# Kernel optimization log

Hardware: AMD Instinct MI355X
Metric: run time of the kernel (lower is better)

Reference implementation:

```python
import jax, jax.numpy as jnp
import numpy as np
from jax import lax

HIDDEN = 16
DN = ('NCHW', 'OIHW', 'NCHW')

def setup_inputs() -> dict:
    key = jax.random.key(0)
    k1, k2, k3 = jax.random.split(key, 3)
    b, t, c, h, w = 8, 12, 5, 256, 256
    x = jax.random.normal(k1, (b, t, c, h, w), dtype=jnp.float32)
    # PyTorch-like init scale for conv weights
    W_cell = jax.random.normal(k2, (4 * HIDDEN, c + HIDDEN, 3, 3), dtype=jnp.float32) * 0.05
    b_cell = jnp.zeros((4 * HIDDEN,), dtype=jnp.float32)
    W_final = jax.random.normal(k3, (1, HIDDEN, 1, 1), dtype=jnp.float32) * 0.1
    b_final = jnp.zeros((1,), dtype=jnp.float32)
    return {"x": x, "W_cell": W_cell, "b_cell": b_cell,
            "W_final": W_final, "b_final": b_final}

def _cell_step(h_c, x_t, W_cell, b_cell):
    h_cur, c_cur = h_c
    combined = jnp.concatenate([x_t, h_cur], axis=1)          # [B, C+H, H, W]
    conv = lax.conv_general_dilated(combined, W_cell, (1, 1), 'SAME',
                                    dimension_numbers=DN)
    conv = conv + b_cell[None, :, None, None]                  # [B, 4H, H, W]
    cc_i, cc_f, cc_o, cc_g = jnp.split(conv, 4, axis=1)
    i = jax.nn.sigmoid(cc_i)
    f = jax.nn.sigmoid(cc_f)
    o = jax.nn.sigmoid(cc_o)
    g = jnp.tanh(cc_g)
    c_next = f * c_cur + i * g
    h_next = o * jnp.tanh(c_next)
    return h_next, c_next

def reference(x, W_cell, b_cell, W_final, b_final):
    b, t, c, hh, ww = x.shape
    h0 = jnp.zeros((b, HIDDEN, hh, ww), dtype=x.dtype)
    c0 = jnp.zeros((b, HIDDEN, hh, ww), dtype=x.dtype)
    xt = jnp.moveaxis(x, 1, 0)  # [T, B, C, H, W] for scan over time

    def step(carry, x_t):
        return _cell_step(carry, x_t, W_cell, b_cell), None

    (h_last, _), _ = lax.scan(step, (h0, c0), xt)
    out = lax.conv_general_dilated(h_last, W_final, (1, 1), 'SAME',
                                   dimension_numbers=DN)
    out = out + b_final[None, :, None, None]
    return out
```

## Files before the change

kernel.cpp:

```cpp
#include <hip/hip_runtime.h>
#include <math.h>

#define HIDDEN 16
#define CIN 5
#define BB 8
#define TT 12
#define HH 256
#define WW 256
#define TX 32
#define TY 8
#define HALO_X 34
#define HALO_Y 10
#define NPX (HALO_X * HALO_Y)
#define STRIDE 40

typedef __attribute__((ext_vector_type(8))) short bf16x8;
typedef __attribute__((ext_vector_type(4))) float floatx4;

__device__ __forceinline__ unsigned short f2bf(float f) {
    unsigned int u = __float_as_uint(f);
    u += 0x7fffu + ((u >> 16) & 1u);
    return (unsigned short)(u >> 16);
}
__device__ __forceinline__ float bf2f(unsigned short s) {
    return __uint_as_float(((unsigned int)s) << 16);
}
__device__ __forceinline__ float fast_sigmoid(float x) { return 1.0f / (1.0f + __expf(-x)); }
__device__ __forceinline__ float fast_tanh(float x) {
    float e2 = __expf(-2.0f * fabsf(x));
    float t = (1.0f - e2) / (1.0f + e2);
    return copysignf(t, x);
}

__global__ void prep_w_kernel(const float* __restrict__ Wc,
                              unsigned short* __restrict__ Wfrag) {
    int i = blockIdx.x * 256 + threadIdx.x;
    if (i >= 9 * 4 * 64 * 8) return;
    int j    = i & 7;
    int lane = (i >> 3) & 63;
    int g    = (i >> 9) & 3;
    int tap  = i >> 11;
    int k    = ((lane >> 4) << 3) + j;
    int col  = lane & 15;
    int o    = g * 16 + col;
    float w  = 0.0f;
    if (k < 21) {
        int ci_ref = (k < 16) ? (5 + k) : (k - 16);
        w = Wc[(o * 21 + ci_ref) * 9 + tap];
    }
    Wfrag[i] = f2bf(w);
}

__global__ void prep_x_kernel(const float* __restrict__ x,
                              unsigned short* __restrict__ xp) {
    size_t n = (size_t)blockIdx.x * 256 + threadIdx.x;
    const size_t TOTPX = (size_t)BB * TT * HH * WW;
    if (n >= TOTPX) return;
    size_t bt  = n / (size_t)(HH * WW);
    size_t pix = n - bt * (size_t)(HH * WW);
    const float* src = x + bt * (size_t)CIN * HH * WW + pix;
    unsigned short v[8];
    #pragma unroll
    for (int c = 0; c < CIN; ++c) v[c] = f2bf(src[(size_t)c * HH * WW]);
    v[5] = 0; v[6] = 0; v[7] = 0;
    *(uint4*)&xp[n * 8] = *(const uint4*)v;
}

__global__ __launch_bounds__(256, 5)
void convlstm_step_kernel(const float* __restrict__ x, int t,
                          const unsigned short* __restrict__ xp,
                          const unsigned short* __restrict__ h_in,
                          unsigned short* __restrict__ h_out,
                          float* __restrict__ c_state,
                          const unsigned short* __restrict__ Wfrag,
                          const float* __restrict__ bias,
                          int first, int use_xp) {
    __shared__ unsigned short tile[NPX * STRIDE];

    const int tid  = threadIdx.x;
    const int lane = tid & 63;
    const int wave = tid >> 6;
    const int x0 = blockIdx.x * TX;
    const int y0 = blockIdx.y * TY;
    const int bb = blockIdx.z;

    for (int i = tid; i < NPX; i += 256) {
        int ly = i / HALO_X;
        int lx = i - ly * HALO_X;
        int gy = y0 + ly - 1;
        int gx = x0 + lx - 1;
        bool inb = (gy >= 0 && gy < HH && gx >= 0 && gx < WW);
        unsigned short* row = &tile[i * STRIDE];
        uint4 z = {0, 0, 0, 0};
        if (inb && !first) {
            size_t hb = ((size_t)bb * HH * WW + (size_t)gy * WW + gx) * HIDDEN;
            *(uint4*)&row[0] = *(const uint4*)&h_in[hb];
            *(uint4*)&row[8] = *(const uint4*)&h_in[hb + 8];
        } else {
            *(uint4*)&row[0] = z;
            *(uint4*)&row[8] = z;
        }
        if (use_xp) {
            if (inb) {
                size_t xb = (((size_t)bb * TT + t) * (size_t)(HH * WW)
                             + (size_t)gy * WW + gx) * 8;
                *(uint4*)&row[16] = *(const uint4*)&xp[xb];
            } else {
                *(uint4*)&row[16] = z;
            }
        } else {
            #pragma unroll
            for (int ci = 0; ci < CIN; ++ci) {
                float v = 0.0f;
                if (inb) v = x[(((size_t)bb * TT + t) * CIN + ci) * (size_t)(HH * WW)
                               + (size_t)gy * WW + gx];
                row[16 + ci] = f2bf(v);
            }
            row[21] = 0; row[22] = 0; row[23] = 0;
        }
        *(uint4*)&row[24] = z;
    }
    __syncthreads();

    const int u    = lane & 15;
    const int quad = lane >> 4;

    float bg[4];
    #pragma unroll
    for (int g = 0; g < 4; ++g) bg[g] = bias[g * 16 + u];

    #pragma unroll 1
    for (int half = 0; half < 2; ++half) {
        floatx4 acc[2][4];
        int abase[2];
        #pragma unroll
        for (int mh = 0; mh < 2; ++mh) {
            int ml = half * 2 + mh;
            int m  = wave + ml * 4;
            int my = m >> 1;
            int mx = (m & 1) << 4;
            abase[mh] = (my * HALO_X + mx + u) * STRIDE + quad * 8;
            #pragma unroll
            for (int g = 0; g < 4; ++g)
                acc[mh][g] = (floatx4){bg[g], bg[g], bg[g], bg[g]};
        }

        #pragma unroll 3
        for (int tap = 0; tap < 9; ++tap) {
            int ky = tap / 3;
            int kx = tap - ky * 3;
            int toff = (ky * HALO_X + kx) * STRIDE;
            bf16x8 bfr[4];
            #pragma unroll
            for (int g = 0; g < 4; ++g)
                bfr[g] = *(const bf16x8*)&Wfrag[(size_t)((tap * 4 + g) * 64 + lane) * 8];
            #pragma unroll
            for (int mh = 0; mh < 2; ++mh) {
                bf16x8 af = *(const bf16x8*)&tile[abase[mh] + toff];
                #pragma unroll
                for (int g = 0; g < 4; ++g)
                    acc[mh][g] = __builtin_amdgcn_mfma_f32_16x16x32_bf16(
                        af, bfr[g], acc[mh][g], 0, 0, 0);
            }
        }

        #pragma unroll
        for (int mh = 0; mh < 2; ++mh) {
            int ml = half * 2 + mh;
            int m  = wave + ml * 4;
            int my = m >> 1;
            int mx = (m & 1) << 4;
            int py = y0 + my;
            #pragma unroll
            for (int r = 0; r < 4; ++r) {
                int pxx = x0 + mx + quad * 4 + r;
                size_t idx = ((size_t)bb * HH * WW + (size_t)py * WW + pxx) * HIDDEN + u;
                float ig = fast_sigmoid(acc[mh][0][r]);
                float fg = fast_sigmoid(acc[mh][1][r]);
                float og = fast_sigmoid(acc[mh][2][r]);
                float gg = fast_tanh(acc[mh][3][r]);
                float c_old = first ? 0.0f : c_state[idx];
                float c_new = fg * c_old + ig * gg;
                c_state[idx] = c_new;
                h_out[idx] = f2bf(og * fast_tanh(c_new));
            }
        }
    }
}

__global__ void final_conv_kernel(const unsigned short* __restrict__ h,
                                  const float* __restrict__ Wf,
                                  const float* __restrict__ bf_,
                                  float* __restrict__ out) {
    int i = blockIdx.x * 256 + threadIdx.x;
    if (i >= BB * HH * WW) return;
    size_t base = (size_t)i * HIDDEN;
    uint4 v0 = *(const uint4*)&h[base];
    uint4 v1 = *(const uint4*)&h[base + 8];
    const unsigned short* p0 = (const unsigned short*)&v0;
    const unsigned short* p1 = (const unsigned short*)&v1;
    float s = bf_[0];
    #pragma unroll
    for (int k = 0; k < 8; ++k) s += Wf[k] * bf2f(p0[k]);
    #pragma unroll
    for (int k = 0; k < 8; ++k) s += Wf[8 + k] * bf2f(p1[k]);
    out[i] = s;
}

extern "C" void kernel_launch(void* const* d_in, const int* in_sizes, int n_in,
                              void* d_out, int out_size, void* d_ws, size_t ws_size,
                              hipStream_t stream) {
    const float* x  = (const float*)d_in[0];
    const float* Wc = (const float*)d_in[1];
    const float* bc = (const float*)d_in[2];
    const float* Wf = (const float*)d_in[3];
    const float* bf = (const float*)d_in[4];
    float* out = (float*)d_out;

    char* ws = (char*)d_ws;
    const size_t h_bytes = (size_t)BB * HH * WW * HIDDEN * 2;
    const size_t c_bytes = (size_t)BB * HH * WW * HIDDEN * 4;
    const size_t w_bytes = 9 * 4 * 64 * 8 * 2;
    const size_t x_bytes = (size_t)BB * TT * HH * WW * 8 * 2;

    unsigned short* h_a = (unsigned short*)(ws);
    unsigned short* h_b = (unsigned short*)(ws + h_bytes);
    float* c            = (float*)(ws + 2 * h_bytes);
    unsigned short* Wfr = (unsigned short*)(ws + 2 * h_bytes + c_bytes);
    unsigned short* xp  = (unsigned short*)(ws + 2 * h_bytes + c_bytes + w_bytes);

    const int use_xp =
        (ws_size >= 2 * h_bytes + c_bytes + w_bytes + x_bytes) ? 1 : 0;

    prep_w_kernel<<<(9 * 4 * 64 * 8 + 255) / 256, 256, 0, stream>>>(Wc, Wfr);
    if (use_xp) {
        size_t totpx = (size_t)BB * TT * HH * WW;
        prep_x_kernel<<<(int)((totpx + 255) / 256), 256, 0, stream>>>(x, xp);
    }

    dim3 grid(WW / TX, HH / TY, BB);
    dim3 block(256, 1, 1);

    const unsigned short* h_in = h_a;
    for (int t = 0; t < TT; ++t) {
        unsigned short* h_out = (t & 1) ? h_b : h_a;
        convlstm_step_kernel<<<grid, block, 0, stream>>>(
            x, t, use_xp ? xp : (const unsigned short*)0,
            h_in, h_out, c, Wfr, bc, (t == 0) ? 1 : 0, use_xp);
        h_in = h_out;
    }

    final_conv_kernel<<<(BB * HH * WW + 255) / 256, 256, 0, stream>>>(
        h_in, Wf, bf, out);
}
```

Measured before the change: 695.9 us.

## Pack conv K dimension across taps to cut MFMA count from 9 to 7

Repacks the implicit-GEMM reduction so each 32-wide MFMA K slice spans two taps of hidden channels (16 each) or several taps of the 5 input channels, instead of one tap padded from 21 to 32. This drops the per-tile MFMA count per output group from 9 to 7 and removes wasted zero-padded K lanes. The cost is irregular per-quad LDS offsets, including one special slot at offset 70*STRIDE that is meant to point at a zero region. Both the weight packing and the A-fragment addressing must match exactly for the result to stay correct.

```diff
diff --git a/kernel.cpp b/kernel.cpp
--- a/kernel.cpp
+++ b/kernel.cpp
@@ -13,6 +13,7 @@
 #define HALO_Y 10
 #define NPX (HALO_X * HALO_Y)
 #define STRIDE 40
+#define NMFMA 7
 
 typedef __attribute__((ext_vector_type(8))) short bf16x8;
 typedef __attribute__((ext_vector_type(4))) float floatx4;
@@ -35,18 +36,25 @@
 __global__ void prep_w_kernel(const float* __restrict__ Wc,
                               unsigned short* __restrict__ Wfrag) {
     int i = blockIdx.x * 256 + threadIdx.x;
-    if (i >= 9 * 4 * 64 * 8) return;
+    if (i >= NMFMA * 4 * 64 * 8) return;
     int j    = i & 7;
     int lane = (i >> 3) & 63;
     int g    = (i >> 9) & 3;
-    int tap  = i >> 11;
+    int mi   = i >> 11;
     int k    = ((lane >> 4) << 3) + j;
     int col  = lane & 15;
     int o    = g * 16 + col;
+    int slot = 2 * mi + (k >> 4);
+    int w16  = k & 15;
     float w  = 0.0f;
-    if (k < 21) {
-        int ci_ref = (k < 16) ? (5 + k) : (k - 16);
-        w = Wc[(o * 21 + ci_ref) * 9 + tap];
+    if (slot <= 8) {
+        w = Wc[(o * 21 + 5 + w16) * 9 + slot];
+    } else {
+        int pair = slot - 9;
+        int xt   = pair * 2 + (w16 >> 3);
+        int ch   = w16 & 7;
+        if (xt < 9 && ch < 5)
+            w = Wc[(o * 21 + ch) * 9 + xt];
     }
     Wfrag[i] = f2bf(w);
 }
@@ -125,6 +133,20 @@
     const int u    = lane & 15;
     const int quad = lane >> 4;
 
+    int aoff[NMFMA];
+    #pragma unroll
+    for (int s = 0; s < 4; ++s) {
+        int tap = s * 2 + (quad >> 1);
+        aoff[s] = ((tap / 3) * HALO_X + (tap % 3)) * STRIDE + (quad & 1) * 8;
+    }
+    aoff[4] = (quad < 2) ? (70 * STRIDE + quad * 8)
+                         : ((quad - 2) * STRIDE + 16);
+    { int t5 = 2 + quad;
+      aoff[5] = ((t5 / 3) * HALO_X + (t5 % 3)) * STRIDE + 16; }
+    { int t6 = (quad == 3) ? 8 : (6 + quad);
+      int of6 = (quad == 3) ? 24 : 16;
+      aoff[6] = ((t6 / 3) * HALO_X + (t6 % 3)) * STRIDE + of6; }
+
     float bg[4];
     #pragma unroll
     for (int g = 0; g < 4; ++g) bg[g] = bias[g * 16 + u];
@@ -139,24 +161,21 @@
             int m  = wave + ml * 4;
             int my = m >> 1;
             int mx = (m & 1) << 4;
-            abase[mh] = (my * HALO_X + mx + u) * STRIDE + quad * 8;
+            abase[mh] = (my * HALO_X + mx + u) * STRIDE;
             #pragma unroll
             for (int g = 0; g < 4; ++g)
                 acc[mh][g] = (floatx4){bg[g], bg[g], bg[g], bg[g]};
         }
 
-        #pragma unroll 3
-        for (int tap = 0; tap < 9; ++tap) {
-            int ky = tap / 3;
-            int kx = tap - ky * 3;
-            int toff = (ky * HALO_X + kx) * STRIDE;
+        #pragma unroll
+        for (int mi = 0; mi < NMFMA; ++mi) {
             bf16x8 bfr[4];
             #pragma unroll
             for (int g = 0; g < 4; ++g)
-                bfr[g] = *(const bf16x8*)&Wfrag[(size_t)((tap * 4 + g) * 64 + lane) * 8];
+                bfr[g] = *(const bf16x8*)&Wfrag[(size_t)((mi * 4 + g) * 64 + lane) * 8];
             #pragma unroll
             for (int mh = 0; mh < 2; ++mh) {
-                bf16x8 af = *(const bf16x8*)&tile[abase[mh] + toff];
+                bf16x8 af = *(const bf16x8*)&tile[abase[mh] + aoff[mi]];
                 #pragma unroll
                 for (int g = 0; g < 4; ++g)
                     acc[mh][g] = __builtin_amdgcn_mfma_f32_16x16x32_bf16(
@@ -220,7 +239,7 @@
     char* ws = (char*)d_ws;
     const size_t h_bytes = (size_t)BB * HH * WW * HIDDEN * 2;
     const size_t c_bytes = (size_t)BB * HH * WW * HIDDEN * 4;
-    const size_t w_bytes = 9 * 4 * 64 * 8 * 2;
+    const size_t w_bytes = NMFMA * 4 * 64 * 8 * 2;
     const size_t x_bytes = (size_t)BB * TT * HH * WW * 8 * 2;
 
     unsigned short* h_a = (unsigned short*)(ws);
@@ -232,7 +251,7 @@
     const int use_xp =
         (ws_size >= 2 * h_bytes + c_bytes + w_bytes + x_bytes) ? 1 : 0;
 
-    prep_w_kernel<<<(9 * 4 * 64 * 8 + 255) / 256, 256, 0, stream>>>(Wc, Wfr);
+    prep_w_kernel<<<(NMFMA * 4 * 64 * 8 + 255) / 256, 256, 0, stream>>>(Wc, Wfr);
     if (use_xp) {
         size_t totpx = (size_t)BB * TT * HH * WW;
         prep_x_kernel<<<(int)((totpx + 255) / 256), 256, 0, stream>>>(x, xp);
```

Result: slower. 1.665 ms (+139.2%).

## Fuse all timesteps into a persistent cooperative kernel with register-resident cell state

Applied to the files above, without the earlier changes.

Replaces the twelve per-timestep launches and the final conv launch with one cooperative persistent kernel. It runs 1024 blocks that each own two tiles, keeps the cell state c in registers across timesteps, and uses grid.sync between steps. The final 1x1 conv is fused into the last step through a shuffle reduction. This removes launch gaps and the global c-state reads and writes, at the cost of grid-wide barriers, lower occupancy (launch bounds 4), and more register pressure from the eight-float cell arrays per tile.

```diff
diff --git a/kernel.cpp b/kernel.cpp
--- a/kernel.cpp
+++ b/kernel.cpp
@@ -1,4 +1,5 @@
 #include <hip/hip_runtime.h>
+#include <hip/hip_cooperative_groups.h>
 #include <math.h>
 
 #define HIDDEN 16
@@ -13,9 +14,12 @@
 #define HALO_Y 10
 #define NPX (HALO_X * HALO_Y)
 #define STRIDE 40
+#define NBLK_PERSIST 1024
 
 typedef __attribute__((ext_vector_type(8))) short bf16x8;
 typedef __attribute__((ext_vector_type(4))) float floatx4;
+
+namespace cg = cooperative_groups;
 
 __device__ __forceinline__ unsigned short f2bf(float f) {
     unsigned int u = __float_as_uint(f);
@@ -66,6 +70,169 @@
     *(uint4*)&xp[n * 8] = *(const uint4*)v;
 }
 
+__global__ __launch_bounds__(256, 4)
+void convlstm_persistent_kernel(const float* __restrict__ x,
+                                const unsigned short* __restrict__ xp,
+                                unsigned short* __restrict__ ha,
+                                unsigned short* __restrict__ hbuf,
+                                const unsigned short* __restrict__ Wfrag,
+                                const float* __restrict__ bias,
+                                const float* __restrict__ Wf,
+                                const float* __restrict__ bfin,
+                                float* __restrict__ out,
+                                int use_xp) {
+    __shared__ unsigned short tile[NPX * STRIDE];
+    cg::grid_group grid = cg::this_grid();
+
+    const int tid  = threadIdx.x;
+    const int lane = tid & 63;
+    const int wave = tid >> 6;
+    const int u    = lane & 15;
+    const int quad = lane >> 4;
+
+    float bg[4];
+    #pragma unroll
+    for (int g = 0; g < 4; ++g) bg[g] = bias[g * 16 + u];
+    const float wfu = Wf[u];
+    const float bf0 = bfin[0];
+
+    float cA[2][2][4];
+    float cB[2][2][4];
+    #pragma unroll
+    for (int a = 0; a < 2; ++a)
+        #pragma unroll
+        for (int m = 0; m < 2; ++m)
+            #pragma unroll
+            for (int r = 0; r < 4; ++r) { cA[a][m][r] = 0.0f; cB[a][m][r] = 0.0f; }
+
+    #pragma unroll 1
+    for (int t = 0; t < TT; ++t) {
+        const unsigned short* h_in  = (t & 1) ? ha : hbuf;
+        unsigned short*       h_out = (t & 1) ? hbuf : ha;
+        const int first = (t == 0);
+        const int last  = (t == TT - 1);
+
+        #pragma unroll
+        for (int tl = 0; tl < 2; ++tl) {
+            const int n  = (int)blockIdx.x + tl * NBLK_PERSIST;
+            const int x0 = (n & 7) * TX;
+            const int y0 = ((n >> 3) & 31) * TY;
+            const int bb = n >> 8;
+
+            if (t > 0 || tl > 0) __syncthreads();
+
+            for (int i = tid; i < NPX; i += 256) {
+                int ly = i / HALO_X;
+                int lx = i - ly * HALO_X;
+                int gy = y0 + ly - 1;
+                int gx = x0 + lx - 1;
+                bool inb = (gy >= 0 && gy < HH && gx >= 0 && gx < WW);
+                unsigned short* row = &tile[i * STRIDE];
+                uint4 z = {0, 0, 0, 0};
+                if (inb && !first) {
+                    size_t hbase = ((size_t)bb * HH * WW + (size_t)gy * WW + gx) * HIDDEN;
+                    *(uint4*)&row[0] = *(const uint4*)&h_in[hbase];
+                    *(uint4*)&row[8] = *(const uint4*)&h_in[hbase + 8];
+                } else {
+                    *(uint4*)&row[0] = z;
+                    *(uint4*)&row[8] = z;
+                }
+                if (use_xp) {
+                    if (inb) {
+                        size_t xb = (((size_t)bb * TT + t) * (size_t)(HH * WW)
+                                     + (size_t)gy * WW + gx) * 8;
+                        *(uint4*)&row[16] = *(const uint4*)&xp[xb];
+                    } else {
+                        *(uint4*)&row[16] = z;
+                    }
+                } else {
+                    #pragma unroll
+                    for (int ci = 0; ci < CIN; ++ci) {
+                        float v = 0.0f;
+                        if (inb) v = x[(((size_t)bb * TT + t) * CIN + ci) * (size_t)(HH * WW)
+                                       + (size_t)gy * WW + gx];
+                        row[16 + ci] = f2bf(v);
+                    }
+                    row[21] = 0; row[22] = 0; row[23] = 0;
+                }
+                *(uint4*)&row[24] = z;
+            }
+            __syncthreads();
+
+            #pragma unroll 1
+            for (int half = 0; half < 2; ++half) {
+                floatx4 acc[2][4];
+                int abase[2];
+                #pragma unroll
+                for (int mh = 0; mh < 2; ++mh) {
+                    int ml = half * 2 + mh;
+                    int m  = wave + ml * 4;
+                    int my = m >> 1;
+                    int mx = (m & 1) << 4;
+                    abase[mh] = (my * HALO_X + mx + u) * STRIDE + quad * 8;
+                    #pragma unroll
+                    for (int g = 0; g < 4; ++g)
+                        acc[mh][g] = (floatx4){bg[g], bg[g], bg[g], bg[g]};
+                }
+
+                #pragma unroll 3
+                for (int tap = 0; tap < 9; ++tap) {
+                    int ky = tap / 3;
+                    int kx = tap - ky * 3;
+                    int toff = (ky * HALO_X + kx) * STRIDE;
+                    bf16x8 bfr[4];
+                    #pragma unroll
+                    for (int g = 0; g < 4; ++g)
+                        bfr[g] = *(const bf16x8*)&Wfrag[(size_t)((tap * 4 + g) * 64 + lane) * 8];
+                    #pragma unroll
+                    for (int mh = 0; mh < 2; ++mh) {
+                        bf16x8 af = *(const bf16x8*)&tile[abase[mh] + toff];
+                        #pragma unroll
+                        for (int g = 0; g < 4; ++g)
+                            acc[mh][g] = __builtin_amdgcn_mfma_f32_16x16x32_bf16(
+                                af, bfr[g], acc[mh][g], 0, 0, 0);
+                    }
+                }
+
+                #pragma unroll
+                for (int mh = 0; mh < 2; ++mh) {
+                    int ml = half * 2 + mh;
+                    int m  = wave + ml * 4;
+                    int my = m >> 1;
+                    int mx = (m & 1) << 4;
+                    int py = y0 + my;
+                    #pragma unroll
+                    for (int r = 0; r < 4; ++r) {
+                        int pxx = x0 + mx + quad * 4 + r;
+                        float ig = fast_sigmoid(acc[mh][0][r]);
+                        float fg = fast_sigmoid(acc[mh][1][r]);
+                        float og = fast_sigmoid(acc[mh][2][r]);
+                        float gg = fast_tanh(acc[mh][3][r]);
+                        float c_old = half ? cB[tl][mh][r] : cA[tl][mh][r];
+                        float c_new = fg * c_old + ig * gg;
+                        if (half) cB[tl][mh][r] = c_new; else cA[tl][mh][r] = c_new;
+                        float hval = og * fast_tanh(c_new);
+                        if (last) {
+                            float s = wfu * hval;
+                            s += __shfl_xor(s, 1);
+                            s += __shfl_xor(s, 2);
+                            s += __shfl_xor(s, 4);
+                            s += __shfl_xor(s, 8);
+                            if (u == 0)
+                                out[(size_t)bb * HH * WW + (size_t)py * WW + pxx] = s + bf0;
+                        } else {
+                            size_t idx = ((size_t)bb * HH * WW + (size_t)py * WW + pxx)
+                                         * HIDDEN + u;
+                            h_out[idx] = f2bf(hval);
+                        }
+                    }
+                }
+            }
+        }
+        if (t != TT - 1) grid.sync();
+    }
+}
+
 __global__ __launch_bounds__(256, 5)
 void convlstm_step_kernel(const float* __restrict__ x, int t,
                           const unsigned short* __restrict__ xp,
@@ -93,9 +260,9 @@
         unsigned short* row = &tile[i * STRIDE];
         uint4 z = {0, 0, 0, 0};
         if (inb && !first) {
-            size_t hb = ((size_t)bb * HH * WW + (size_t)gy * WW + gx) * HIDDEN;
-            *(uint4*)&row[0] = *(const uint4*)&h_in[hb];
-            *(uint4*)&row[8] = *(const uint4*)&h_in[hb + 8];
+            size_t hbase = ((size_t)bb * HH * WW + (size_t)gy * WW + gx) * HIDDEN;
+            *(uint4*)&row[0] = *(const uint4*)&h_in[hbase];
+            *(uint4*)&row[8] = *(const uint4*)&h_in[hbase + 8];
         } else {
             *(uint4*)&row[0] = z;
             *(uint4*)&row[8] = z;
@@ -238,18 +405,36 @@
         prep_x_kernel<<<(int)((totpx + 255) / 256), 256, 0, stream>>>(x, xp);
     }
 
-    dim3 grid(WW / TX, HH / TY, BB);
-    dim3 block(256, 1, 1);
-
-    const unsigned short* h_in = h_a;
-    for (int t = 0; t < TT; ++t) {
-        unsigned short* h_out = (t & 1) ? h_b : h_a;
-        convlstm_step_kernel<<<grid, block, 0, stream>>>(
-            x, t, use_xp ? xp : (const unsigned short*)0,
-            h_in, h_out, c, Wfr, bc, (t == 0) ? 1 : 0, use_xp);
-        h_in = h_out;
-    }
-
-    final_conv_kernel<<<(BB * HH * WW + 255) / 256, 256, 0, stream>>>(
-        h_in, Wf, bf, out);
-}
+    int occ = 0;
+    hipOccupancyMaxActiveBlocksPerMultiprocessor(&occ, convlstm_persistent_kernel,
+                                                 256, 0);
+    bool done = false;
+    if (occ >= 4) {
+        const unsigned short* xp_arg = use_xp ? xp : (const unsigned short*)0;
+        int use_xp_arg = use_xp;
+        void* kargs[] = {
+            (void*)&x, (void*)&xp_arg, (void*)&h_a, (void*)&h_b,
+            (void*)&Wfr, (void*)&bc, (void*)&Wf, (void*)&bf,
+            (void*)&out, (void*)&use_xp_arg
+        };
+        if (hipLaunchCooperativeKernel((const void*)convlstm_persistent_kernel,
+                                       dim3(NBLK_PERSIST, 1, 1), dim3(256, 1, 1),
+                                       kargs, 0, stream) == hipSuccess)
+            done = true;
+    }
+
+    if (!done) {
+        dim3 grid(WW / TX, HH / TY, BB);
+        dim3 block(256, 1, 1);
+        const unsigned short* h_in = h_a;
+        for (int t = 0; t < TT; ++t) {
+            unsigned short* h_out = (t & 1) ? h_b : h_a;
+            convlstm_step_kernel<<<grid, block, 0, stream>>>(
+                x, t, use_xp ? xp : (const unsigned short*)0,
+                h_in, h_out, c, Wfr, bc, (t == 0) ? 1 : 0, use_xp);
+            h_in = h_out;
+        }
+        final_conv_kernel<<<(BB * HH * WW + 255) / 256, 256, 0, stream>>>(
+            h_in, Wf, bf, out);
+    }
+}
```

New measurement: 686.2 us. Within noise of the previous version (-1.4%).
